# Optimization experiments

Hardware: AMD Instinct MI355X
Metric: run time of the kernel (lower is better)

The kernel has to match this reference:

```python
import jax, jax.numpy as jnp
from jax import lax
import numpy as np


def _run_lstm(x, W, U, b, reverse=False):
    # x: [B,T,I]; W: [I,4U]; U: [U,4U]; b: [4U]; Keras gate order i,f,g,o
    # activation='relu' (candidate and cell-output), recurrent_activation=sigmoid
    if reverse:
        x = x[:, ::-1]
    u = U.shape[0]
    xz = jnp.einsum('bti,ij->btj', x, W) + b  # precompute input projection

    def step(carry, z_t):
        h, c = carry
        z = z_t + h @ U
        i, f, g, o = jnp.split(z, 4, axis=-1)
        i = jax.nn.sigmoid(i)
        f = jax.nn.sigmoid(f)
        g = jax.nn.relu(g)
        o = jax.nn.sigmoid(o)
        c = f * c + i * g
        h = o * jax.nn.relu(c)
        return (h, c), h

    B = x.shape[0]
    init = (jnp.zeros((B, u), x.dtype), jnp.zeros((B, u), x.dtype))
    _, hs = lax.scan(step, init, jnp.swapaxes(xz, 0, 1))
    hs = jnp.swapaxes(hs, 0, 1)  # [B,T,U]
    if reverse:
        hs = hs[:, ::-1]  # Keras Bidirectional re-reverses backward output
    return hs


def _bilstm(x, Wf, Uf, bf, Wb, Ub, bb):
    return jnp.concatenate([_run_lstm(x, Wf, Uf, bf, False),
                            _run_lstm(x, Wb, Ub, bb, True)], axis=-1)


def _forward(x, p):
    (e1fW, e1fU, e1fb, e1bW, e1bU, e1bb,
     e2fW, e2fU, e2fb, e2bW, e2bU, e2bb,
     d1fW, d1fU, d1fb, d1bW, d1bU, d1bb,
     d2fW, d2fU, d2fb, d2bW, d2bU, d2bb,
     Wd, bd) = p
    T = x.shape[1]
    h = _bilstm(x, e1fW, e1fU, e1fb, e1bW, e1bU, e1bb)          # [B,T,2N]
    # encoder lstm2: return_sequences=False -> last fwd state, last bwd state
    fwd = _run_lstm(h, e2fW, e2fU, e2fb, False)[:, -1]           # [B,N/2]
    bwd = _run_lstm(h, e2bW, e2bU, e2bb, True)[:, 0]             # [B,N/2]
    z = jnp.concatenate([fwd, bwd], axis=-1)                     # [B,N]
    z = jnp.broadcast_to(z[:, None, :], (z.shape[0], T, z.shape[1]))  # RepeatVector
    h = _bilstm(z, d1fW, d1fU, d1fb, d1bW, d1bU, d1bb)           # [B,T,N]
    h = _bilstm(h, d2fW, d2fU, d2fb, d2bW, d2bU, d2bb)           # [B,T,2N]
    return jnp.einsum('btd,df->btf', h, Wd) + bd                 # TimeDistributed Dense


def setup_inputs():
    B, T, F, N = 512, 256, 64, 128
    ks = iter(jax.random.split(jax.random.key(0), 40))

    def p(shape, s=0.05):
        return jax.random.normal(next(ks), shape, jnp.float32) * s

    def cell(ind, u):
        # Keras defaults: zero bias with unit forget-gate bias
        b = jnp.zeros((4 * u,), jnp.float32).at[u:2 * u].set(1.0)
        return p((ind, 4 * u)), p((u, 4 * u)), b

    d = {'x': jax.random.normal(next(ks), (B, T, F), jnp.float32)}
    for name, ind, u in [('e1', F, N), ('e2', 2 * N, N // 2), ('d1', N, N // 2), ('d2', N, N)]:
        for dr in ('f', 'b'):
            W, U, b = cell(ind, u)
            d[name + dr + '_W'] = W
            d[name + dr + '_U'] = U
            d[name + dr + '_b'] = b
    d['Wd'] = p((2 * N, F))
    d['bd'] = jnp.zeros((F,), jnp.float32)
    return d


def reference(x, e1f_W, e1f_U, e1f_b, e1b_W, e1b_U, e1b_b,
              e2f_W, e2f_U, e2f_b, e2b_W, e2b_U, e2b_b,
              d1f_W, d1f_U, d1f_b, d1b_W, d1b_U, d1b_b,
              d2f_W, d2f_U, d2f_b, d2b_W, d2b_U, d2b_b, Wd, bd):
    return _forward(x, (e1f_W, e1f_U, e1f_b, e1b_W, e1b_U, e1b_b,
                        e2f_W, e2f_U, e2f_b, e2b_W, e2b_U, e2b_b,
                        d1f_W, d1f_U, d1f_b, d1b_W, d1b_U, d1b_b,
                        d2f_W, d2f_U, d2f_b, d2b_W, d2b_U, d2b_b, Wd, bd))
```

## Files before the change

### kernel.cpp

```cpp
#include <hip/hip_runtime.h>


#define THREADS 512

__device__ __forceinline__ float sigf(float x) { return 1.0f / (1.0f + __expf(-x)); }

template<int UH, int CT, int KH, int MODE, bool LASTONLY, int BT>
__global__ __launch_bounds__(THREADS, 2)
void lstm_rec(const float* __restrict__ xin,
              const float* __restrict__ Uf, const float* __restrict__ Ub,
              const float* __restrict__ bf, const float* __restrict__ bb,
              const float* __restrict__ Wf, const float* __restrict__ Wb,
              float* __restrict__ out,
              float* __restrict__ stc, float* __restrict__ sth,
              const int T, const int t0, const int TC, const int FIRST, const int LASTC)
{
    constexpr int NCOL = 4 * UH;
    constexpr int CG   = NCOL / CT;
    constexpr int URPK = UH / KH;
    constexpr int IN   = (MODE == 0) ? 64 : ((MODE == 2) ? 128 : 4);
    constexpr int XRPK = (MODE == 0) ? (IN / KH) : 4;
    constexpr int GT   = BT * UH;
    static_assert(CG == 128 && CG * KH == THREADS, "mapping");
    static_assert(URPK % 4 == 0 && (MODE != 0 || XRPK % 4 == 0), "vec4");
    static_assert(GT <= THREADS, "gate");

    const int dir = blockIdx.y;
    const bool rev = (dir != 0);
    const float* __restrict__ U    = dir ? Ub : Uf;
    const float* __restrict__ Wm   = dir ? Wb : Wf;
    const float* __restrict__ bias = dir ? bb : bf;

    const int b0  = blockIdx.x * BT;
    const int tid = threadIdx.x;
    const int kh  = tid >> 7;
    const int cg  = tid & 127;

    __shared__ float v[BT][UH];
    __shared__ float slab[KH][BT][NCOL];
    __shared__ float xb[BT][IN];

    float wu[CT][URPK];
    #pragma unroll
    for (int j = 0; j < CT; ++j)
        #pragma unroll
        for (int r = 0; r < URPK; ++r)
            wu[j][r] = U[(size_t)(kh * URPK + r) * NCOL + cg + j * CG];

    float wx[CT][XRPK];
    if (MODE == 0) {
        #pragma unroll
        for (int j = 0; j < CT; ++j)
            #pragma unroll
            for (int r = 0; r < XRPK; ++r)
                wx[j][r] = Wm[(size_t)(kh * XRPK + r) * NCOL + cg + j * CG];
    }

    const int gb = tid / UH;
    const int gu = tid % UH;

    float cst = 0.0f, prc[4];
    if (FIRST) {
        for (int i = tid; i < BT * UH; i += THREADS) v[i / UH][i % UH] = 0.0f;
    } else if (tid < GT) {
        cst = stc[((size_t)dir * 512 + b0 + gb) * UH + gu];
        v[gb][gu] = sth[((size_t)dir * 512 + b0 + gb) * UH + gu];
    }
    if (tid < GT) {
        #pragma unroll
        for (int g = 0; g < 4; ++g) prc[g] = bias[g * UH + gu];
    }

    if (MODE == 2) {
        {
            const int b = tid / IN, k = tid % IN;
            xb[b][k] = xin[(size_t)(b0 + b) * IN + k];
        }
        __syncthreads();
        if (tid < GT) {
            for (int k = 0; k < IN; ++k) {
                const float zk = xb[gb][k];
                #pragma unroll
                for (int g = 0; g < 4; ++g)
                    prc[g] = fmaf(zk, Wm[(size_t)k * NCOL + g * UH + gu], prc[g]);
            }
        }
    }

    float hlast = 0.0f;

    for (int p = 0; p < TC; ++p) {
        const int gt = rev ? (T - 1 - (t0 + p)) : (t0 + p);

        float xzp[4];
        if (MODE == 0) {
            if (tid < 64) {
                const int b = tid >> 4, f = (tid & 15) * 4;
                *(float4*)&xb[b][f] =
                    *(const float4*)&xin[((size_t)(b0 + b) * T + gt) * 64 + f];
            }
        } else if (MODE == 1) {
            if (tid < GT) {
                const float* xr = xin + (((size_t)dir * TC + p) * 512 + (b0 + gb)) * NCOL;
                #pragma unroll
                for (int g = 0; g < 4; ++g) xzp[g] = xr[g * UH + gu];
            }
        }
        __syncthreads();

        float acc[CT][BT];
        #pragma unroll
        for (int j = 0; j < CT; ++j)
            #pragma unroll
            for (int b = 0; b < BT; ++b) acc[j][b] = 0.0f;

        if (MODE == 0) {
            #pragma unroll
            for (int r = 0; r < XRPK; r += 4) {
                float4 xv[BT];
                #pragma unroll
                for (int b = 0; b < BT; ++b)
                    xv[b] = *(const float4*)&xb[b][kh * XRPK + r];
                #pragma unroll
                for (int j = 0; j < CT; ++j)
                    #pragma unroll
                    for (int b = 0; b < BT; ++b) {
                        acc[j][b] = fmaf(xv[b].x, wx[j][r + 0], acc[j][b]);
                        acc[j][b] = fmaf(xv[b].y, wx[j][r + 1], acc[j][b]);
                        acc[j][b] = fmaf(xv[b].z, wx[j][r + 2], acc[j][b]);
                        acc[j][b] = fmaf(xv[b].w, wx[j][r + 3], acc[j][b]);
                    }
            }
        }
        #pragma unroll
        for (int r = 0; r < URPK; r += 4) {
            float4 hv[BT];
            #pragma unroll
            for (int b = 0; b < BT; ++b)
                hv[b] = *(const float4*)&v[b][kh * URPK + r];
            #pragma unroll
            for (int j = 0; j < CT; ++j)
                #pragma unroll
                for (int b = 0; b < BT; ++b) {
                    acc[j][b] = fmaf(hv[b].x, wu[j][r + 0], acc[j][b]);
                    acc[j][b] = fmaf(hv[b].y, wu[j][r + 1], acc[j][b]);
                    acc[j][b] = fmaf(hv[b].z, wu[j][r + 2], acc[j][b]);
                    acc[j][b] = fmaf(hv[b].w, wu[j][r + 3], acc[j][b]);
                }
        }
        #pragma unroll
        for (int j = 0; j < CT; ++j)
            #pragma unroll
            for (int b = 0; b < BT; ++b) slab[kh][b][cg + j * CG] = acc[j][b];

        __syncthreads();

        if (tid < GT) {
            float z[4];
            #pragma unroll
            for (int g = 0; g < 4; ++g) {
                z[g] = prc[g];
                if (MODE == 1) z[g] += xzp[g];
                #pragma unroll
                for (int w = 0; w < KH; ++w) z[g] += slab[w][gb][g * UH + gu];
            }
            const float iv = sigf(z[0]);
            const float fv = sigf(z[1]);
            const float gv = fmaxf(z[2], 0.0f);
            const float ov = sigf(z[3]);
            const float c  = fv * cst + iv * gv;
            cst = c;
            const float h = ov * fmaxf(c, 0.0f);
            hlast = h;
            v[gb][gu] = h;
            if (!LASTONLY) {
                out[((size_t)(b0 + gb) * T + gt) * (2 * UH) + (size_t)dir * UH + gu] = h;
            } else if (LASTC && p == TC - 1) {
                out[(size_t)(b0 + gb) * (2 * UH) + (size_t)dir * UH + gu] = h;
            }
        }
    }

    if (tid < GT) {
        stc[((size_t)dir * 512 + b0 + gb) * UH + gu] = cst;
        sth[((size_t)dir * 512 + b0 + gb) * UH + gu] = hlast;
    }
}

template<int K, int NCOL>
__global__ __launch_bounds__(256, 2)
void xz_gemm(const float* __restrict__ A,
             const float* __restrict__ Wf, const float* __restrict__ Wb,
             float* __restrict__ xz, const int T, const int t0, const int TC)
{
    const int dir = blockIdx.z;
    const float* __restrict__ W = dir ? Wb : Wf;
    const int row0 = blockIdx.x * 64;
    const int col0 = blockIdx.y * 64;
    const int tid = threadIdx.x;
    const int tx = tid & 15, ty = tid >> 4;

    __shared__ float As[64][17];
    __shared__ float Bs[16][64];

    float acc[4][4];
    #pragma unroll
    for (int i = 0; i < 4; ++i)
        #pragma unroll
        for (int j = 0; j < 4; ++j) acc[i][j] = 0.0f;

    const int r_st  = tid >> 2;
    const int kq    = (tid & 3) * 4;
    const int rowA  = row0 + r_st;
    const int ltA   = rowA >> 9, bA = rowA & 511;
    const int gtA   = dir ? (T - 1 - (t0 + ltA)) : (t0 + ltA);
    const float* Arow = A + ((size_t)bA * T + gtA) * K;
    const int kr = tid >> 4, c4 = (tid & 15) * 4;

    for (int kc = 0; kc < K; kc += 16) {
        *(float4*)&As[r_st][kq] = *(const float4*)&Arow[kc + kq];
        *(float4*)&Bs[kr][c4]   = *(const float4*)&W[(size_t)(kc + kr) * NCOL + col0 + c4];
        __syncthreads();
        #pragma unroll
        for (int kk = 0; kk < 16; ++kk) {
            float a[4];
            #pragma unroll
            for (int i = 0; i < 4; ++i) a[i] = As[ty * 4 + i][kk];
            const float4 bv = *(const float4*)&Bs[kk][tx * 4];
            #pragma unroll
            for (int i = 0; i < 4; ++i) {
                acc[i][0] = fmaf(a[i], bv.x, acc[i][0]);
                acc[i][1] = fmaf(a[i], bv.y, acc[i][1]);
                acc[i][2] = fmaf(a[i], bv.z, acc[i][2]);
                acc[i][3] = fmaf(a[i], bv.w, acc[i][3]);
            }
        }
        __syncthreads();
    }
    #pragma unroll
    for (int i = 0; i < 4; ++i) {
        const int row = row0 + ty * 4 + i;
        const int lt = row >> 9, b = row & 511;
        float4 o; o.x = acc[i][0]; o.y = acc[i][1]; o.z = acc[i][2]; o.w = acc[i][3];
        *(float4*)&xz[(((size_t)dir * TC + lt) * 512 + b) * NCOL + col0 + tx * 4] = o;
    }
}

__global__ __launch_bounds__(256, 1)
void dense_out(const float* __restrict__ h, const float* __restrict__ Wd,
               const float* __restrict__ bd, float* __restrict__ out, const int rows)
{
    const int tid = threadIdx.x;
    const int lc  = (tid & 15) * 4;
    const size_t row = (size_t)blockIdx.x * 16 + (tid >> 4);
    if (row >= (size_t)rows) return;
    const float* hr = h + row * 256;
    float4 a;
    a.x = bd[lc]; a.y = bd[lc + 1]; a.z = bd[lc + 2]; a.w = bd[lc + 3];
    #pragma unroll 4
    for (int k = 0; k < 256; k += 4) {
        const float4 hv = *reinterpret_cast<const float4*>(&hr[k]);
        const float4 w0 = *reinterpret_cast<const float4*>(&Wd[(size_t)(k + 0) * 64 + lc]);
        const float4 w1 = *reinterpret_cast<const float4*>(&Wd[(size_t)(k + 1) * 64 + lc]);
        const float4 w2 = *reinterpret_cast<const float4*>(&Wd[(size_t)(k + 2) * 64 + lc]);
        const float4 w3 = *reinterpret_cast<const float4*>(&Wd[(size_t)(k + 3) * 64 + lc]);
        a.x = fmaf(hv.x, w0.x, a.x); a.y = fmaf(hv.x, w0.y, a.y); a.z = fmaf(hv.x, w0.z, a.z); a.w = fmaf(hv.x, w0.w, a.w);
        a.x = fmaf(hv.y, w1.x, a.x); a.y = fmaf(hv.y, w1.y, a.y); a.z = fmaf(hv.y, w1.z, a.z); a.w = fmaf(hv.y, w1.w, a.w);
        a.x = fmaf(hv.z, w2.x, a.x); a.y = fmaf(hv.z, w2.y, a.y); a.z = fmaf(hv.z, w2.z, a.z); a.w = fmaf(hv.z, w2.w, a.w);
        a.x = fmaf(hv.w, w3.x, a.x); a.y = fmaf(hv.w, w3.y, a.y); a.z = fmaf(hv.w, w3.z, a.z); a.w = fmaf(hv.w, w3.w, a.w);
    }
    *reinterpret_cast<float4*>(&out[row * 64 + lc]) = a;
}

extern "C" void kernel_launch(void* const* d_in, const int* in_sizes, int n_in,
                              void* d_out, int out_size, void* d_ws, size_t ws_size,
                              hipStream_t stream)
{
    (void)in_sizes; (void)n_in; (void)out_size;
    constexpr int B = 512, T = 256, BT = 4;

    const size_t n_h1 = (size_t)B * T * 256;
    const size_t n_h2 = (size_t)B * T * 128;
    const size_t n_z  = (size_t)B * 128;
    const size_t n_st = 2 * ((size_t)2 * B * 64) + 2 * ((size_t)2 * B * 128);
    const size_t base = n_h1 + n_h2 + n_z + n_st;
    int TC = 0;
    for (int tc : {64, 32, 16}) {
        if ((base + (size_t)tc * 2 * B * 512) * sizeof(float) <= ws_size) { TC = tc; break; }
    }
    if (!TC) return;
    const int NCH = T / TC;

    const float* x    = (const float*)d_in[0];
    const float* e1fW = (const float*)d_in[1];
    const float* e1fU = (const float*)d_in[2];
    const float* e1fb = (const float*)d_in[3];
    const float* e1bW = (const float*)d_in[4];
    const float* e1bU = (const float*)d_in[5];
    const float* e1bb = (const float*)d_in[6];
    const float* e2fW = (const float*)d_in[7];
    const float* e2fU = (const float*)d_in[8];
    const float* e2fb = (const float*)d_in[9];
    const float* e2bW = (const float*)d_in[10];
    const float* e2bU = (const float*)d_in[11];
    const float* e2bb = (const float*)d_in[12];
    const float* d1fW = (const float*)d_in[13];
    const float* d1fU = (const float*)d_in[14];
    const float* d1fb = (const float*)d_in[15];
    const float* d1bW = (const float*)d_in[16];
    const float* d1bU = (const float*)d_in[17];
    const float* d1bb = (const float*)d_in[18];
    const float* d2fW = (const float*)d_in[19];
    const float* d2fU = (const float*)d_in[20];
    const float* d2fb = (const float*)d_in[21];
    const float* d2bW = (const float*)d_in[22];
    const float* d2bU = (const float*)d_in[23];
    const float* d2bb = (const float*)d_in[24];
    const float* Wd   = (const float*)d_in[25];
    const float* bd   = (const float*)d_in[26];
    float* out = (float*)d_out;

    float* ws   = (float*)d_ws;
    float* h1   = ws;
    float* h2   = h1 + n_h1;
    float* zv   = h2 + n_h2;
    float* st   = zv + n_z;
    float* stcE = st;
    float* sthE = stcE + (size_t)2 * B * 64;
    float* stcD = sthE + (size_t)2 * B * 64;
    float* sthD = stcD + (size_t)2 * B * 128;
    float* xzb  = st + n_st;
    float* h3   = h1;

    const dim3 rgrid(B / BT, 2), rblk(THREADS);

    lstm_rec<128, 4, 4, 0, false, BT><<<rgrid, rblk, 0, stream>>>(
        x, e1fU, e1bU, e1fb, e1bb, e1fW, e1bW, h1, stcD, sthD, T, 0, T, 1, 1);

    for (int c = 0; c < NCH; ++c) {
        xz_gemm<256, 256><<<dim3(TC * B / 64, 256 / 64, 2), 256, 0, stream>>>(
            h1, e2fW, e2bW, xzb, T, c * TC, TC);
        lstm_rec<64, 2, 4, 1, true, BT><<<rgrid, rblk, 0, stream>>>(
            xzb, e2fU, e2bU, e2fb, e2bb, nullptr, nullptr, zv, stcE, sthE,
            T, c * TC, TC, c == 0, c == NCH - 1);
    }

    lstm_rec<64, 2, 4, 2, false, BT><<<rgrid, rblk, 0, stream>>>(
        zv, d1fU, d1bU, d1fb, d1bb, d1fW, d1bW, h2, stcE, sthE, T, 0, T, 1, 1);

    for (int c = 0; c < NCH; ++c) {
        xz_gemm<128, 512><<<dim3(TC * B / 64, 512 / 64, 2), 256, 0, stream>>>(
            h2, d2fW, d2bW, xzb, T, c * TC, TC);
        lstm_rec<128, 4, 4, 1, false, BT><<<rgrid, rblk, 0, stream>>>(
            xzb, d2fU, d2bU, d2fb, d2bb, nullptr, nullptr, h3, stcD, sthD,
            T, c * TC, TC, c == 0, c == NCH - 1);
    }

    dense_out<<<(B * T + 15) / 16, 256, 0, stream>>>(h3, Wd, bd, out, B * T);
}
```

Measured before the change: 3.132 ms.

## Run LSTM recurrence on bf16 MFMA with split hi/lo precision and 16-row tiles

Rewrites the recurrent kernel so the h@U product uses bf16 MFMA instructions. Weights and hidden state are split into hi and lo bf16 parts, and three MFMAs per tile recover near-fp32 accuracy. Each block now handles 16 batch rows instead of 4, and the first-layer input projection is double-buffered in LDS via MFMA. The bias add moves into the xz GEMM, and the decoder's constant-input projection is computed once by a GEMM. The goal is to cut the scalar FMA cost of the sequential recurrence, at the price of three MFMAs per tile and some residual precision loss.

Result: slower. 3.389 ms (+8.2%).

```diff
diff --git a/kernel.cpp b/kernel.cpp
--- a/kernel.cpp
+++ b/kernel.cpp
@@ -3,198 +3,241 @@
 
 #define THREADS 512
 
+using f32x4 = __attribute__((ext_vector_type(4))) float;
+using bfrag = __attribute__((ext_vector_type(8))) short;
+
 __device__ __forceinline__ float sigf(float x) { return 1.0f / (1.0f + __expf(-x)); }
-
-template<int UH, int CT, int KH, int MODE, bool LASTONLY, int BT>
+__device__ __forceinline__ unsigned short f2bf(float f) {
+    unsigned u = __float_as_uint(f);
+    u += 0x7FFFu + ((u >> 16) & 1u);
+    return (unsigned short)(u >> 16);
+}
+__device__ __forceinline__ float bf2f(unsigned short h) {
+    return __uint_as_float(((unsigned)h) << 16);
+}
+__device__ __forceinline__ int fragw(int kc, int r) {
+    return ((kc * 16 + r) ^ (kc & 7)) * 8;
+}
+
+template<int UH, int XK, bool LASTONLY>
 __global__ __launch_bounds__(THREADS, 2)
-void lstm_rec(const float* __restrict__ xin,
+void lstm_rec(const float* __restrict__ xz, const size_t xz_ds, const size_t xz_ss,
+              const float* __restrict__ xin,
               const float* __restrict__ Uf, const float* __restrict__ Ub,
+              const float* __restrict__ Wf, const float* __restrict__ Wb,
               const float* __restrict__ bf, const float* __restrict__ bb,
-              const float* __restrict__ Wf, const float* __restrict__ Wb,
               float* __restrict__ out,
               float* __restrict__ stc, float* __restrict__ sth,
-              const int T, const int t0, const int TC, const int FIRST, const int LASTC)
+              const int T, const int t0, const int TCc, const int FIRST, const int LASTC)
 {
     constexpr int NCOL = 4 * UH;
-    constexpr int CG   = NCOL / CT;
-    constexpr int URPK = UH / KH;
-    constexpr int IN   = (MODE == 0) ? 64 : ((MODE == 2) ? 128 : 4);
-    constexpr int XRPK = (MODE == 0) ? (IN / KH) : 4;
-    constexpr int GT   = BT * UH;
-    static_assert(CG == 128 && CG * KH == THREADS, "mapping");
-    static_assert(URPK % 4 == 0 && (MODE != 0 || XRPK % 4 == 0), "vec4");
-    static_assert(GT <= THREADS, "gate");
+    constexpr int NS   = NCOL / 8;
+    constexpr int NT   = NS / 16;
+    constexpr int KT   = UH / 32;
+    constexpr int XKT  = XK / 32;
+    constexpr int PPT  = 16 * UH / THREADS;
+    constexpr int BQS  = THREADS / UH;
+    constexpr int ZP   = NCOL + 4;
+    static_assert(XK == 0 || XK == 64, "x path");
+    static_assert(NT >= 1 && KT >= 1 && PPT >= 1, "shape");
 
     const int dir = blockIdx.y;
     const bool rev = (dir != 0);
-    const float* __restrict__ U    = dir ? Ub : Uf;
-    const float* __restrict__ Wm   = dir ? Wb : Wf;
-    const float* __restrict__ bias = dir ? bb : bf;
-
-    const int b0  = blockIdx.x * BT;
+    const float* __restrict__ U  = dir ? Ub : Uf;
+    const float* __restrict__ Wm = dir ? Wb : Wf;
+    const float* __restrict__ bs = dir ? bb : bf;
+
+    const int b0  = blockIdx.x * 16;
     const int tid = threadIdx.x;
-    const int kh  = tid >> 7;
-    const int cg  = tid & 127;
-
-    __shared__ float v[BT][UH];
-    __shared__ float slab[KH][BT][NCOL];
-    __shared__ float xb[BT][IN];
-
-    float wu[CT][URPK];
+    const int wv  = tid >> 6;
+    const int l   = tid & 63;
+    const int lr  = l & 15;
+    const int kg  = l >> 4;
+    const int c0  = wv * NS;
+
+    __shared__ unsigned short hh_hi[UH * 16], hh_lo[UH * 16];
+    __shared__ unsigned short xh_hi[XK > 0 ? 2 * XK * 16 : 8];
+    __shared__ unsigned short xh_lo[XK > 0 ? 2 * XK * 16 : 8];
+    __shared__ float zs[16 * ZP];
+
+    bfrag whi[NT][KT], wlo[NT][KT];
     #pragma unroll
-    for (int j = 0; j < CT; ++j)
-        #pragma unroll
-        for (int r = 0; r < URPK; ++r)
-            wu[j][r] = U[(size_t)(kh * URPK + r) * NCOL + cg + j * CG];
-
-    float wx[CT][XRPK];
-    if (MODE == 0) {
-        #pragma unroll
-        for (int j = 0; j < CT; ++j)
-            #pragma unroll
-            for (int r = 0; r < XRPK; ++r)
-                wx[j][r] = Wm[(size_t)(kh * XRPK + r) * NCOL + cg + j * CG];
-    }
-
-    const int gb = tid / UH;
-    const int gu = tid % UH;
-
-    float cst = 0.0f, prc[4];
+    for (int nt = 0; nt < NT; ++nt)
+        #pragma unroll
+        for (int kt = 0; kt < KT; ++kt) {
+            const int col = c0 + nt * 16 + lr;
+            #pragma unroll
+            for (int i = 0; i < 8; ++i) {
+                const int k = kt * 32 + kg * 8 + i;
+                const float w = U[(size_t)k * NCOL + col];
+                const unsigned short h = f2bf(w);
+                whi[nt][kt][i] = (short)h;
+                wlo[nt][kt][i] = (short)f2bf(w - bf2f(h));
+            }
+        }
+    bfrag wxhi[NT][XKT > 0 ? XKT : 1];
+    float biasr[NT];
+    if constexpr (XK > 0) {
+        #pragma unroll
+        for (int nt = 0; nt < NT; ++nt) {
+            const int col = c0 + nt * 16 + lr;
+            #pragma unroll
+            for (int kt = 0; kt < XKT; ++kt)
+                #pragma unroll
+                for (int i = 0; i < 8; ++i)
+                    wxhi[nt][kt][i] = (short)f2bf(Wm[(size_t)(kt * 32 + kg * 8 + i) * NCOL + col]);
+            biasr[nt] = bs[col];
+        }
+    }
+
+    const int ut = tid % UH;
+    float cst[PPT];
+
     if (FIRST) {
-        for (int i = tid; i < BT * UH; i += THREADS) v[i / UH][i % UH] = 0.0f;
-    } else if (tid < GT) {
-        cst = stc[((size_t)dir * 512 + b0 + gb) * UH + gu];
-        v[gb][gu] = sth[((size_t)dir * 512 + b0 + gb) * UH + gu];
-    }
-    if (tid < GT) {
-        #pragma unroll
-        for (int g = 0; g < 4; ++g) prc[g] = bias[g * UH + gu];
-    }
-
-    if (MODE == 2) {
-        {
-            const int b = tid / IN, k = tid % IN;
-            xb[b][k] = xin[(size_t)(b0 + b) * IN + k];
-        }
+        for (int i = tid; i < UH * 16; i += THREADS) { hh_hi[i] = 0; hh_lo[i] = 0; }
+        #pragma unroll
+        for (int q = 0; q < PPT; ++q) cst[q] = 0.0f;
+    } else {
+        #pragma unroll
+        for (int q = 0; q < PPT; ++q) {
+            const int b = tid / UH + q * BQS;
+            const float hv = sth[((size_t)dir * 512 + b0 + b) * UH + ut];
+            const unsigned short hi = f2bf(hv);
+            const unsigned short lo = f2bf(hv - bf2f(hi));
+            hh_hi[fragw(ut >> 3, b) + (ut & 7)] = hi;
+            hh_lo[fragw(ut >> 3, b) + (ut & 7)] = lo;
+            cst[q] = stc[((size_t)dir * 512 + b0 + b) * UH + ut];
+        }
+    }
+    if constexpr (XK > 0) {
+        const int gt0 = rev ? (T - 1 - t0) : t0;
+        const int bb = tid >> 5, f = (tid & 31) * 2;
+        const float2 xv = *(const float2*)&xin[((size_t)(b0 + bb) * T + gt0) * XK + f];
+        const unsigned short h0 = f2bf(xv.x), h1 = f2bf(xv.y);
+        const unsigned short l0 = f2bf(xv.x - bf2f(h0)), l1 = f2bf(xv.y - bf2f(h1));
+        const int off = fragw(f >> 3, bb) + (f & 7);
+        *(unsigned*)&xh_hi[off] = (unsigned)h0 | ((unsigned)h1 << 16);
+        *(unsigned*)&xh_lo[off] = (unsigned)l0 | ((unsigned)l1 << 16);
+    }
+    __syncthreads();
+
+    for (int p = 0; p < TCc; ++p) {
+        const int gt = rev ? (T - 1 - (t0 + p)) : (t0 + p);
+
+        float2 xnext;
+        const bool havex = (XK > 0) && (p + 1 < TCc);
+        if (havex) {
+            const int gtn = rev ? (T - 1 - (t0 + p + 1)) : (t0 + p + 1);
+            const int bb = tid >> 5, f = (tid & 31) * 2;
+            xnext = *(const float2*)&xin[((size_t)(b0 + bb) * T + gtn) * XK + f];
+        }
+        float xzr[PPT][4];
+        if constexpr (XK == 0) {
+            const float* xrow = xz + (size_t)dir * xz_ds + (size_t)p * xz_ss;
+            #pragma unroll
+            for (int q = 0; q < PPT; ++q) {
+                const int b = tid / UH + q * BQS;
+                const float* r = xrow + (size_t)(b0 + b) * NCOL + ut;
+                #pragma unroll
+                for (int g = 0; g < 4; ++g) xzr[q][g] = r[g * UH];
+            }
+        }
+
+        f32x4 acc[NT];
+        #pragma unroll
+        for (int nt = 0; nt < NT; ++nt) {
+            if constexpr (XK > 0) acc[nt] = f32x4{biasr[nt], biasr[nt], biasr[nt], biasr[nt]};
+            else                  acc[nt] = f32x4{0.f, 0.f, 0.f, 0.f};
+        }
+        #pragma unroll
+        for (int kt = 0; kt < KT; ++kt) {
+            const bfrag ahi = *(const bfrag*)&hh_hi[fragw(kt * 4 + kg, lr)];
+            const bfrag alo = *(const bfrag*)&hh_lo[fragw(kt * 4 + kg, lr)];
+            #pragma unroll
+            for (int nt = 0; nt < NT; ++nt) {
+                acc[nt] = __builtin_amdgcn_mfma_f32_16x16x32_bf16(ahi, whi[nt][kt], acc[nt], 0, 0, 0);
+                acc[nt] = __builtin_amdgcn_mfma_f32_16x16x32_bf16(alo, whi[nt][kt], acc[nt], 0, 0, 0);
+                acc[nt] = __builtin_amdgcn_mfma_f32_16x16x32_bf16(ahi, wlo[nt][kt], acc[nt], 0, 0, 0);
+            }
+        }
+        if constexpr (XK > 0) {
+            const int xb = (p & 1) * XK * 16;
+            #pragma unroll
+            for (int kt = 0; kt < XKT; ++kt) {
+                const bfrag xhi = *(const bfrag*)&xh_hi[xb + fragw(kt * 4 + kg, lr)];
+                const bfrag xlo = *(const bfrag*)&xh_lo[xb + fragw(kt * 4 + kg, lr)];
+                #pragma unroll
+                for (int nt = 0; nt < NT; ++nt) {
+                    acc[nt] = __builtin_amdgcn_mfma_f32_16x16x32_bf16(xhi, wxhi[nt][kt], acc[nt], 0, 0, 0);
+                    acc[nt] = __builtin_amdgcn_mfma_f32_16x16x32_bf16(xlo, wxhi[nt][kt], acc[nt], 0, 0, 0);
+                }
+            }
+        }
+        #pragma unroll
+        for (int nt = 0; nt < NT; ++nt)
+            #pragma unroll
+            for (int qq = 0; qq < 4; ++qq)
+                zs[(kg * 4 + qq) * ZP + c0 + nt * 16 + lr] = acc[nt][qq];
+
         __syncthreads();
-        if (tid < GT) {
-            for (int k = 0; k < IN; ++k) {
-                const float zk = xb[gb][k];
-                #pragma unroll
-                for (int g = 0; g < 4; ++g)
-                    prc[g] = fmaf(zk, Wm[(size_t)k * NCOL + g * UH + gu], prc[g]);
-            }
-        }
-    }
-
-    float hlast = 0.0f;
-
-    for (int p = 0; p < TC; ++p) {
-        const int gt = rev ? (T - 1 - (t0 + p)) : (t0 + p);
-
-        float xzp[4];
-        if (MODE == 0) {
-            if (tid < 64) {
-                const int b = tid >> 4, f = (tid & 15) * 4;
-                *(float4*)&xb[b][f] =
-                    *(const float4*)&xin[((size_t)(b0 + b) * T + gt) * 64 + f];
-            }
-        } else if (MODE == 1) {
-            if (tid < GT) {
-                const float* xr = xin + (((size_t)dir * TC + p) * 512 + (b0 + gb)) * NCOL;
-                #pragma unroll
-                for (int g = 0; g < 4; ++g) xzp[g] = xr[g * UH + gu];
-            }
+
+        if (havex) {
+            const int bb = tid >> 5, f = (tid & 31) * 2;
+            const unsigned short h0 = f2bf(xnext.x), h1 = f2bf(xnext.y);
+            const unsigned short l0 = f2bf(xnext.x - bf2f(h0)), l1 = f2bf(xnext.y - bf2f(h1));
+            const int off = ((p + 1) & 1) * XK * 16 + fragw(f >> 3, bb) + (f & 7);
+            *(unsigned*)&xh_hi[off] = (unsigned)h0 | ((unsigned)h1 << 16);
+            *(unsigned*)&xh_lo[off] = (unsigned)l0 | ((unsigned)l1 << 16);
+        }
+
+        #pragma unroll
+        for (int q = 0; q < PPT; ++q) {
+            const int b = tid / UH + q * BQS;
+            float z0 = zs[b * ZP + 0 * UH + ut];
+            float z1 = zs[b * ZP + 1 * UH + ut];
+            float z2 = zs[b * ZP + 2 * UH + ut];
+            float z3 = zs[b * ZP + 3 * UH + ut];
+            if constexpr (XK == 0) { z0 += xzr[q][0]; z1 += xzr[q][1]; z2 += xzr[q][2]; z3 += xzr[q][3]; }
+            const float iv = sigf(z0);
+            const float fv = sigf(z1);
+            const float gv = fmaxf(z2, 0.0f);
+            const float ov = sigf(z3);
+            const float c  = fv * cst[q] + iv * gv;
+            cst[q] = c;
+            const float h = ov * fmaxf(c, 0.0f);
+            if (!LASTONLY) {
+                out[((size_t)(b0 + b) * T + gt) * (2 * UH) + (size_t)dir * UH + ut] = h;
+            } else if (LASTC && p == TCc - 1) {
+                out[(size_t)(b0 + b) * (2 * UH) + (size_t)dir * UH + ut] = h;
+            }
+            const unsigned short hi = f2bf(h);
+            const unsigned short lo = f2bf(h - bf2f(hi));
+            hh_hi[fragw(ut >> 3, b) + (ut & 7)] = hi;
+            hh_lo[fragw(ut >> 3, b) + (ut & 7)] = lo;
         }
         __syncthreads();
-
-        float acc[CT][BT];
-        #pragma unroll
-        for (int j = 0; j < CT; ++j)
-            #pragma unroll
-            for (int b = 0; b < BT; ++b) acc[j][b] = 0.0f;
-
-        if (MODE == 0) {
-            #pragma unroll
-            for (int r = 0; r < XRPK; r += 4) {
-                float4 xv[BT];
-                #pragma unroll
-                for (int b = 0; b < BT; ++b)
-                    xv[b] = *(const float4*)&xb[b][kh * XRPK + r];
-                #pragma unroll
-                for (int j = 0; j < CT; ++j)
-                    #pragma unroll
-                    for (int b = 0; b < BT; ++b) {
-                        acc[j][b] = fmaf(xv[b].x, wx[j][r + 0], acc[j][b]);
-                        acc[j][b] = fmaf(xv[b].y, wx[j][r + 1], acc[j][b]);
-                        acc[j][b] = fmaf(xv[b].z, wx[j][r + 2], acc[j][b]);
-                        acc[j][b] = fmaf(xv[b].w, wx[j][r + 3], acc[j][b]);
-                    }
-            }
-        }
-        #pragma unroll
-        for (int r = 0; r < URPK; r += 4) {
-            float4 hv[BT];
-            #pragma unroll
-            for (int b = 0; b < BT; ++b)
-                hv[b] = *(const float4*)&v[b][kh * URPK + r];
-            #pragma unroll
-            for (int j = 0; j < CT; ++j)
-                #pragma unroll
-                for (int b = 0; b < BT; ++b) {
-                    acc[j][b] = fmaf(hv[b].x, wu[j][r + 0], acc[j][b]);
-                    acc[j][b] = fmaf(hv[b].y, wu[j][r + 1], acc[j][b]);
-                    acc[j][b] = fmaf(hv[b].z, wu[j][r + 2], acc[j][b]);
-                    acc[j][b] = fmaf(hv[b].w, wu[j][r + 3], acc[j][b]);
-                }
-        }
-        #pragma unroll
-        for (int j = 0; j < CT; ++j)
-            #pragma unroll
-            for (int b = 0; b < BT; ++b) slab[kh][b][cg + j * CG] = acc[j][b];
-
-        __syncthreads();
-
-        if (tid < GT) {
-            float z[4];
-            #pragma unroll
-            for (int g = 0; g < 4; ++g) {
-                z[g] = prc[g];
-                if (MODE == 1) z[g] += xzp[g];
-                #pragma unroll
-                for (int w = 0; w < KH; ++w) z[g] += slab[w][gb][g * UH + gu];
-            }
-            const float iv = sigf(z[0]);
-            const float fv = sigf(z[1]);
-            const float gv = fmaxf(z[2], 0.0f);
-            const float ov = sigf(z[3]);
-            const float c  = fv * cst + iv * gv;
-            cst = c;
-            const float h = ov * fmaxf(c, 0.0f);
-            hlast = h;
-            v[gb][gu] = h;
-            if (!LASTONLY) {
-                out[((size_t)(b0 + gb) * T + gt) * (2 * UH) + (size_t)dir * UH + gu] = h;
-            } else if (LASTC && p == TC - 1) {
-                out[(size_t)(b0 + gb) * (2 * UH) + (size_t)dir * UH + gu] = h;
-            }
-        }
-    }
-
-    if (tid < GT) {
-        stc[((size_t)dir * 512 + b0 + gb) * UH + gu] = cst;
-        sth[((size_t)dir * 512 + b0 + gb) * UH + gu] = hlast;
-    }
-}
-
-template<int K, int NCOL>
+    }
+
+    #pragma unroll
+    for (int q = 0; q < PPT; ++q) {
+        const int b = tid / UH + q * BQS;
+        const float hv = bf2f(hh_hi[fragw(ut >> 3, b) + (ut & 7)])
+                       + bf2f(hh_lo[fragw(ut >> 3, b) + (ut & 7)]);
+        sth[((size_t)dir * 512 + b0 + b) * UH + ut] = hv;
+        stc[((size_t)dir * 512 + b0 + b) * UH + ut] = cst[q];
+    }
+}
+
+template<int K, int NC, bool TMAP>
 __global__ __launch_bounds__(256, 2)
 void xz_gemm(const float* __restrict__ A,
              const float* __restrict__ Wf, const float* __restrict__ Wb,
+             const float* __restrict__ bf, const float* __restrict__ bb,
              float* __restrict__ xz, const int T, const int t0, const int TC)
 {
     const int dir = blockIdx.z;
     const float* __restrict__ W = dir ? Wb : Wf;
+    const float* __restrict__ bs = dir ? bb : bf;
     const int row0 = blockIdx.x * 64;
     const int col0 = blockIdx.y * 64;
     const int tid = threadIdx.x;
@@ -209,17 +252,22 @@
         #pragma unroll
         for (int j = 0; j < 4; ++j) acc[i][j] = 0.0f;
 
-    const int r_st  = tid >> 2;
-    const int kq    = (tid & 3) * 4;
-    const int rowA  = row0 + r_st;
-    const int ltA   = rowA >> 9, bA = rowA & 511;
-    const int gtA   = dir ? (T - 1 - (t0 + ltA)) : (t0 + ltA);
-    const float* Arow = A + ((size_t)bA * T + gtA) * K;
+    const int r_st = tid >> 2;
+    const int kq   = (tid & 3) * 4;
+    const int rowA = row0 + r_st;
+    const float* Arow;
+    if (TMAP) {
+        const int ltA = rowA >> 9, bA = rowA & 511;
+        const int gtA = dir ? (T - 1 - (t0 + ltA)) : (t0 + ltA);
+        Arow = A + ((size_t)bA * T + gtA) * K;
+    } else {
+        Arow = A + (size_t)rowA * K;
+    }
     const int kr = tid >> 4, c4 = (tid & 15) * 4;
 
     for (int kc = 0; kc < K; kc += 16) {
         *(float4*)&As[r_st][kq] = *(const float4*)&Arow[kc + kq];
-        *(float4*)&Bs[kr][c4]   = *(const float4*)&W[(size_t)(kc + kr) * NCOL + col0 + c4];
+        *(float4*)&Bs[kr][c4]   = *(const float4*)&W[(size_t)(kc + kr) * NC + col0 + c4];
         __syncthreads();
         #pragma unroll
         for (int kk = 0; kk < 16; ++kk) {
@@ -237,12 +285,19 @@
         }
         __syncthreads();
     }
+    const float4 bv = *(const float4*)&bs[col0 + tx * 4];
     #pragma unroll
     for (int i = 0; i < 4; ++i) {
         const int row = row0 + ty * 4 + i;
-        const int lt = row >> 9, b = row & 511;
-        float4 o; o.x = acc[i][0]; o.y = acc[i][1]; o.z = acc[i][2]; o.w = acc[i][3];
-        *(float4*)&xz[(((size_t)dir * TC + lt) * 512 + b) * NCOL + col0 + tx * 4] = o;
+        float4 o;
+        o.x = acc[i][0] + bv.x; o.y = acc[i][1] + bv.y;
+        o.z = acc[i][2] + bv.z; o.w = acc[i][3] + bv.w;
+        if (TMAP) {
+            const int lt = row >> 9, b = row & 511;
+            *(float4*)&xz[(((size_t)dir * TC + lt) * 512 + b) * NC + col0 + tx * 4] = o;
+        } else {
+            *(float4*)&xz[((size_t)dir * 512 + row) * NC + col0 + tx * 4] = o;
+        }
     }
 }
 
@@ -277,7 +332,7 @@
                               hipStream_t stream)
 {
     (void)in_sizes; (void)n_in; (void)out_size;
-    constexpr int B = 512, T = 256, BT = 4;
+    constexpr int B = 512, T = 256;
 
     const size_t n_h1 = (size_t)B * T * 256;
     const size_t n_h2 = (size_t)B * T * 128;
@@ -330,30 +385,38 @@
     float* stcD = sthE + (size_t)2 * B * 64;
     float* sthD = stcD + (size_t)2 * B * 128;
     float* xzb  = st + n_st;
+    float* xzd1 = xzb;
     float* h3   = h1;
 
-    const dim3 rgrid(B / BT, 2), rblk(THREADS);
-
-    lstm_rec<128, 4, 4, 0, false, BT><<<rgrid, rblk, 0, stream>>>(
-        x, e1fU, e1bU, e1fb, e1bb, e1fW, e1bW, h1, stcD, sthD, T, 0, T, 1, 1);
+    const dim3 rgrid(B / 16, 2), rblk(THREADS);
+
+    lstm_rec<128, 64, false><<<rgrid, rblk, 0, stream>>>(
+        nullptr, 0, 0, x, e1fU, e1bU, e1fW, e1bW, e1fb, e1bb,
+        h1, stcD, sthD, T, 0, T, 1, 1);
 
     for (int c = 0; c < NCH; ++c) {
-        xz_gemm<256, 256><<<dim3(TC * B / 64, 256 / 64, 2), 256, 0, stream>>>(
-            h1, e2fW, e2bW, xzb, T, c * TC, TC);
-        lstm_rec<64, 2, 4, 1, true, BT><<<rgrid, rblk, 0, stream>>>(
-            xzb, e2fU, e2bU, e2fb, e2bb, nullptr, nullptr, zv, stcE, sthE,
-            T, c * TC, TC, c == 0, c == NCH - 1);
-    }
-
-    lstm_rec<64, 2, 4, 2, false, BT><<<rgrid, rblk, 0, stream>>>(
-        zv, d1fU, d1bU, d1fb, d1bb, d1fW, d1bW, h2, stcE, sthE, T, 0, T, 1, 1);
+        xz_gemm<256, 256, true><<<dim3(TC * B / 64, 256 / 64, 2), 256, 0, stream>>>(
+            h1, e2fW, e2bW, e2fb, e2bb, xzb, T, c * TC, TC);
+        lstm_rec<64, 0, true><<<rgrid, rblk, 0, stream>>>(
+            xzb, (size_t)TC * 512 * 256, (size_t)512 * 256, nullptr,
+            e2fU, e2bU, nullptr, nullptr, nullptr, nullptr,
+            zv, stcE, sthE, T, c * TC, TC, c == 0, c == NCH - 1);
+    }
+
+    xz_gemm<128, 256, false><<<dim3(B / 64, 256 / 64, 2), 256, 0, stream>>>(
+        zv, d1fW, d1bW, d1fb, d1bb, xzd1, T, 0, 1);
+    lstm_rec<64, 0, false><<<rgrid, rblk, 0, stream>>>(
+        xzd1, (size_t)512 * 256, 0, nullptr,
+        d1fU, d1bU, nullptr, nullptr, nullptr, nullptr,
+        h2, stcE, sthE, T, 0, T, 1, 1);
 
     for (int c = 0; c < NCH; ++c) {
-        xz_gemm<128, 512><<<dim3(TC * B / 64, 512 / 64, 2), 256, 0, stream>>>(
-            h2, d2fW, d2bW, xzb, T, c * TC, TC);
-        lstm_rec<128, 4, 4, 1, false, BT><<<rgrid, rblk, 0, stream>>>(
-            xzb, d2fU, d2bU, d2fb, d2bb, nullptr, nullptr, h3, stcD, sthD,
-            T, c * TC, TC, c == 0, c == NCH - 1);
+        xz_gemm<128, 512, true><<<dim3(TC * B / 64, 512 / 64, 2), 256, 0, stream>>>(
+            h2, d2fW, d2bW, d2fb, d2bb, xzb, T, c * TC, TC);
+        lstm_rec<128, 0, false><<<rgrid, rblk, 0, stream>>>(
+            xzb, (size_t)TC * 512 * 512, (size_t)512 * 512, nullptr,
+            d2fU, d2bU, nullptr, nullptr, nullptr, nullptr,
+            h3, stcD, sthD, T, c * TC, TC, c == 0, c == NCH - 1);
     }
 
     dense_out<<<(B * T + 15) / 16, 256, 0, stream>>>(h3, Wd, bd, out, B * T);
```
